# Kernel tuning notes

Measured on AMD Instinct MI355X. Metric: run time of the kernel, lower is better.

The kernel has to match this reference:

```python
import jax, jax.numpy as jnp
import numpy as np

N = 131072
D = 512        # input_dim
H = 512        # hidden_dim
E = 10         # num_experts
INIT_STD_SCALE = 0.1


def _trunc_normal(key, shape, std):
    # approximate trunc_normal_(std=std) in [-2std, 2std]
    return jnp.clip(jax.random.normal(key, shape) * std, -2.0 * std, 2.0 * std).astype(jnp.float32)


def setup_inputs() -> dict:
    key = jax.random.key(0)
    ks = jax.random.split(key, 6)
    x = jax.random.normal(ks[0], (N, D), dtype=jnp.float32)
    # router (default nn.Linear init approximated with uniform)
    lim = 1.0 / np.sqrt(D)
    Wr = jax.random.uniform(ks[1], (E, D), minval=-lim, maxval=lim, dtype=jnp.float32)
    br = jnp.zeros((E,), dtype=jnp.float32)
    # experts: trunc_normal with std = 0.1 / sqrt(fan_in), zero bias
    W1 = _trunc_normal(ks[2], (E, D, H), INIT_STD_SCALE / np.sqrt(D))   # [E, D, H]
    b1 = jnp.zeros((E, H), dtype=jnp.float32)
    W2 = _trunc_normal(ks[3], (E, H, H), INIT_STD_SCALE / np.sqrt(H))   # [E, H, H]
    b2 = jnp.zeros((E, H), dtype=jnp.float32)
    return {"x": x, "Wr": Wr, "br": br, "W1": W1, "b1": b1, "W2": W2, "b2": b2}


def reference(x, Wr, br, W1, b1, W2, b2):
    # router in fp32 (autocast disabled in original)
    logits = x.astype(jnp.float32) @ Wr.T + br          # [N, E]
    expert_ids = jnp.argmax(logits, axis=1)              # [N]
    out = jnp.zeros((x.shape[0], W2.shape[-1]), dtype=x.dtype)
    # fixed small loop over experts; dropout is identity at inference
    for e in range(W1.shape[0]):
        h = jax.nn.relu(x @ W1[e] + b1[e])                # [N, H]
        o = h @ W2[e] + b2[e]                             # [N, H]
        out = jnp.where((expert_ids == e)[:, None], o, out)
    return out, expert_ids
```

## Files before the change

### kernel.cpp

```cpp
#include <hip/hip_runtime.h>
#include <hip/hip_bf16.h>

#define N_TOK 131072
#define DIM   512
#define HID   512
#define NEXP  10

using bf16x8 = __attribute__((ext_vector_type(8))) short;
using f32x4  = __attribute__((ext_vector_type(4))) float;

__device__ __forceinline__ short f2bf(float f) {
    union { float f; unsigned u; } v; v.f = f;
    unsigned u = v.u;
    return (short)((u + 0x7FFFu + ((u >> 16) & 1u)) >> 16);
}

#define GLOAD16(g, l) __builtin_amdgcn_global_load_lds( \
    (const __attribute__((address_space(1))) void*)(g),  \
    (__attribute__((address_space(3))) void*)(l), 16, 0, 0)

__global__ __launch_bounds__(256) void router_kernel(
    const float* __restrict__ x, const float* __restrict__ Wr,
    const float* __restrict__ br, int* __restrict__ eid,
    float* __restrict__ ids_out, int* __restrict__ counts,
    short* __restrict__ xb)
{
    __shared__ float wr[NEXP][DIM];
    __shared__ int lcnt[NEXP];
    int tid = threadIdx.x;
    for (int i = tid; i < NEXP * DIM / 4; i += 256)
        ((float4*)wr)[i] = ((const float4*)Wr)[i];
    if (tid < NEXP) lcnt[tid] = 0;
    __syncthreads();

    int lane  = tid & 63;
    int wave  = tid >> 6;
    int gwave = blockIdx.x * 4 + wave;
    int nwav  = gridDim.x * 4;

    for (int t = gwave; t < N_TOK; t += nwav) {
        const float4* xr = (const float4*)(x + (size_t)t * DIM);
        float4 v0 = xr[lane * 2], v1 = xr[lane * 2 + 1];
        float xf[8] = {v0.x, v0.y, v0.z, v0.w, v1.x, v1.y, v1.z, v1.w};
        bf16x8 p;
        #pragma unroll
        for (int j = 0; j < 8; ++j) p[j] = f2bf(xf[j]);
        *(bf16x8*)(xb + (size_t)t * DIM + lane * 8) = p;

        float dot[NEXP];
        #pragma unroll
        for (int e = 0; e < NEXP; ++e) {
            const float* wv = &wr[e][lane * 8];
            float s = 0.f;
            #pragma unroll
            for (int j = 0; j < 8; ++j) s = fmaf(xf[j], wv[j], s);
            dot[e] = s;
        }
        #pragma unroll
        for (int off = 32; off > 0; off >>= 1) {
            #pragma unroll
            for (int e = 0; e < NEXP; ++e) dot[e] += __shfl_xor(dot[e], off, 64);
        }
        if (lane == 0) {
            int best = 0; float bv = dot[0] + br[0];
            #pragma unroll
            for (int e = 1; e < NEXP; ++e) {
                float v = dot[e] + br[e];
                if (v > bv) { bv = v; best = e; }
            }
            eid[t] = best;
            ids_out[t] = (float)best;
            atomicAdd(&lcnt[best], 1);
        }
    }
    __syncthreads();
    if (tid < NEXP) atomicAdd(&counts[tid], lcnt[tid]);
}

__global__ void offsets_kernel(const int* __restrict__ counts,
                               int* __restrict__ offsets, int* __restrict__ toff)
{
    if (threadIdx.x == 0) {
        int acc = 0, ta = 0;
        for (int e = 0; e < NEXP; ++e) {
            offsets[e] = acc; toff[e] = ta;
            acc += counts[e]; ta += (counts[e] + 127) >> 7;
        }
        offsets[NEXP] = acc; toff[NEXP] = ta;
    }
}

__global__ __launch_bounds__(256) void scatter_kernel(
    const int* __restrict__ eid, const int* __restrict__ offsets,
    int* __restrict__ cursors, int* __restrict__ perm)
{
    __shared__ int lcnt[NEXP], lbase[NEXP];
    int tid = threadIdx.x;
    if (tid < NEXP) lcnt[tid] = 0;
    __syncthreads();
    int t = blockIdx.x * 256 + tid;
    int e = 0, lpos = 0;
    if (t < N_TOK) {
        e = eid[t];
        lpos = atomicAdd(&lcnt[e], 1);
    }
    __syncthreads();
    if (tid < NEXP) lbase[tid] = atomicAdd(&cursors[tid], lcnt[tid]);
    __syncthreads();
    if (t < N_TOK) perm[offsets[e] + lbase[e] + lpos] = t;
}

__global__ __launch_bounds__(256) void wconvert_kernel(
    const float* __restrict__ W1, const float* __restrict__ W2,
    short* __restrict__ W1b, short* __restrict__ W2b)
{
    int mat = blockIdx.z;
    const float* src = (mat < NEXP) ? W1 + (size_t)mat * 512 * 512
                                    : W2 + (size_t)(mat - NEXP) * 512 * 512;
    short* dst = (mat < NEXP) ? W1b + (size_t)mat * 512 * 512
                              : W2b + (size_t)(mat - NEXP) * 512 * 512;
    __shared__ float tile[64][65];
    int r0 = blockIdx.y * 64, c0 = blockIdx.x * 64;
    int tid = threadIdx.x;
    int tr = tid >> 4, tc4 = (tid & 15) * 4;
    #pragma unroll
    for (int i = 0; i < 4; ++i) {
        float4 v = *(const float4*)(src + (size_t)(r0 + i * 16 + tr) * 512 + c0 + tc4);
        tile[i * 16 + tr][tc4 + 0] = v.x; tile[i * 16 + tr][tc4 + 1] = v.y;
        tile[i * 16 + tr][tc4 + 2] = v.z; tile[i * 16 + tr][tc4 + 3] = v.w;
    }
    __syncthreads();
    int s   = (r0 + tc4) >> 5;
    int kin = (r0 + tc4) & 31;
    #pragma unroll
    for (int i = 0; i < 4; ++i) {
        int cc = i * 16 + tr;
        ushort4 o;
        o.x = (ushort)f2bf(tile[tc4 + 0][cc]); o.y = (ushort)f2bf(tile[tc4 + 1][cc]);
        o.z = (ushort)f2bf(tile[tc4 + 2][cc]); o.w = (ushort)f2bf(tile[tc4 + 3][cc]);
        *(ushort4*)(dst + (size_t)s * 16384 + (size_t)(c0 + cc) * 32 + kin) = o;
    }
}

template<int LAYER>
__global__ __launch_bounds__(512, 4) void expert_gemm(
    const short* __restrict__ xb, const short* __restrict__ hA,
    const short* __restrict__ WT, const float* __restrict__ bias,
    const int* __restrict__ offsets, const int* __restrict__ toff,
    const int* __restrict__ perm,
    short* __restrict__ hOut, float* __restrict__ out)
{
    int g = blockIdx.x;
    if (g >= toff[NEXP]) return;
    int e = 0;
    #pragma unroll
    for (int k = 1; k < NEXP; ++k) e += (g >= toff[k]);
    int beg = offsets[e], cnt = offsets[e + 1] - beg;
    int m0 = (g - toff[e]) * 128;
    int nb = blockIdx.y * 256;

    __shared__ int toks[128];
    __shared__ short Ab[2][128 * 32];
    __shared__ short Bb[2][256 * 32];

    int tid = threadIdx.x, lane = tid & 63, w = tid >> 6;
    if (tid < 128) toks[tid] = perm[beg + min(m0 + tid, cnt - 1)];
    __syncthreads();

    const short* WTe = WT + (size_t)e * 512 * 512;
    int srow = w * 16 + (lane >> 2);
    int kqp  = lane & 3;
    int ql   = kqp ^ ((srow >> 1) & 3);
    const short* aS;
    if (LAYER == 1) aS = xb + (size_t)toks[srow] * DIM + ql * 8;
    else            aS = hA + (size_t)(beg + min(m0 + srow, cnt - 1)) * HID + ql * 8;
    const short* bS = WTe + (size_t)(nb + srow) * 32 + ql * 8;

    auto stage = [&](int t, int b) {
        GLOAD16(bS + t * 16384,        (char*)&Bb[b][0] + w * 1024);
        GLOAD16(bS + t * 16384 + 4096, (char*)&Bb[b][0] + 8192 + w * 1024);
        GLOAD16(aS + t * 32,           (char*)&Ab[b][0] + w * 1024);
    };

    int wr = w >> 2, wc = w & 3, lrow = lane & 15, kq = lane >> 4;
    int offA[4], offB[4];
    #pragma unroll
    for (int i = 0; i < 4; ++i) {
        int r = wr * 64 + i * 16 + lrow;
        offA[i] = r * 64 + (kq ^ ((r >> 1) & 3)) * 16;
    }
    #pragma unroll
    for (int j = 0; j < 4; ++j) {
        int r = wc * 64 + j * 16 + lrow;
        offB[j] = r * 64 + (kq ^ ((r >> 1) & 3)) * 16;
    }

    f32x4 acc[4][4];
    #pragma unroll
    for (int i = 0; i < 4; ++i)
        #pragma unroll
        for (int j = 0; j < 4; ++j) acc[i][j] = (f32x4){0.f, 0.f, 0.f, 0.f};

    auto comp = [&](int b) {
        bf16x8 af[4], bv[4];
        #pragma unroll
        for (int i = 0; i < 4; ++i) af[i] = *(const bf16x8*)((char*)&Ab[b][0] + offA[i]);
        #pragma unroll
        for (int j = 0; j < 4; ++j) bv[j] = *(const bf16x8*)((char*)&Bb[b][0] + offB[j]);
        __builtin_amdgcn_s_setprio(1);
        #pragma unroll
        for (int i = 0; i < 4; ++i)
            #pragma unroll
            for (int j = 0; j < 4; ++j)
                acc[i][j] = __builtin_amdgcn_mfma_f32_16x16x32_bf16(af[i], bv[j], acc[i][j], 0, 0, 0);
        __builtin_amdgcn_s_setprio(0);
    };

    stage(0, 0);
    stage(1, 1);
    asm volatile("s_waitcnt vmcnt(3)" ::: "memory");
    __builtin_amdgcn_s_barrier();

    #pragma unroll
    for (int t = 0; t < 16; ++t) {
        comp(t & 1);
        if (t == 15) break;
        __builtin_amdgcn_s_barrier();
        asm volatile("" ::: "memory");
        if (t + 2 < 16) {
            stage(t + 2, t & 1);
            asm volatile("s_waitcnt vmcnt(3)" ::: "memory");
        } else {
            asm volatile("s_waitcnt vmcnt(0)" ::: "memory");
        }
        __builtin_amdgcn_s_barrier();
    }

    const float* be = bias + (size_t)e * 512;
    int colb = nb + wc * 64 + lrow;
    float bvv[4];
    #pragma unroll
    for (int j = 0; j < 4; ++j) bvv[j] = be[colb + j * 16];

    #pragma unroll
    for (int i = 0; i < 4; ++i) {
        #pragma unroll
        for (int q = 0; q < 4; ++q) {
            int rr = wr * 64 + i * 16 + kq * 4 + q;
            if (m0 + rr < cnt) {
                if (LAYER == 1) {
                    short* hp = hOut + (size_t)(beg + m0 + rr) * HID + colb;
                    #pragma unroll
                    for (int j = 0; j < 4; ++j) {
                        float v = acc[i][j][q] + bvv[j];
                        hp[j * 16] = f2bf(v > 0.f ? v : 0.f);
                    }
                } else {
                    float* op = out + (size_t)toks[rr] * HID + colb;
                    #pragma unroll
                    for (int j = 0; j < 4; ++j)
                        op[j * 16] = acc[i][j][q] + bvv[j];
                }
            }
        }
    }
}

extern "C" void kernel_launch(void* const* d_in, const int* in_sizes, int n_in,
                              void* d_out, int out_size, void* d_ws, size_t ws_size,
                              hipStream_t stream)
{
    const float* x  = (const float*)d_in[0];
    const float* Wr = (const float*)d_in[1];
    const float* br = (const float*)d_in[2];
    const float* W1 = (const float*)d_in[3];
    const float* b1 = (const float*)d_in[4];
    const float* W2 = (const float*)d_in[5];
    const float* b2 = (const float*)d_in[6];

    float* out     = (float*)d_out;
    float* ids_out = out + (size_t)N_TOK * HID;

    char* ws     = (char*)d_ws;
    int* counts  = (int*)ws;
    int* offsets = counts + 16;
    int* toff    = counts + 32;
    int* cursors = counts + 48;
    int* eid     = (int*)(ws + 1024);
    int* perm    = eid + N_TOK;
    short* W1b   = (short*)(ws + 1024 + (size_t)2 * N_TOK * 4);
    short* W2b   = W1b + (size_t)NEXP * 512 * 512;
    short* h     = W2b + (size_t)NEXP * 512 * 512;
    short* xb    = h   + (size_t)N_TOK * HID;

    hipMemsetAsync(d_ws, 0, 1024, stream);
    router_kernel<<<2048, 256, 0, stream>>>(x, Wr, br, eid, ids_out, counts, xb);
    wconvert_kernel<<<dim3(8, 8, 2 * NEXP), 256, 0, stream>>>(W1, W2, W1b, W2b);
    offsets_kernel<<<1, 64, 0, stream>>>(counts, offsets, toff);
    scatter_kernel<<<512, 256, 0, stream>>>(eid, offsets, cursors, perm);

    int ntiles = (N_TOK + 127) / 128 + NEXP;
    expert_gemm<1><<<dim3(ntiles, 2), 512, 0, stream>>>(xb, nullptr, W1b, b1, offsets, toff, perm, h, nullptr);
    expert_gemm<2><<<dim3(ntiles, 2), 512, 0, stream>>>(nullptr, h, W2b, b2, offsets, toff, perm, nullptr, out);
}
```

Baseline: 366.5 us.

## Fuse both expert GEMM layers into one kernel keeping hidden tile in LDS

Replaces the two per-layer expert GEMM launches with a single fused kernel. Each block computes a 128-token by 256-column slice of the hidden activation, writes it after bias and ReLU into swizzled shared memory, and immediately uses it as the A operand for the second GEMM. Two output accumulator sets cover all 512 output columns. This removes the global write and re-read of the bf16 hidden tensor. The cost is about 112KB of shared memory per block, three accumulator sets raising register pressure (launch bounds drop to 2 blocks per CU), and half as many blocks in the grid. Layer-1 x tiles are also reloaded once per hidden half.

```diff
diff --git a/kernel.cpp b/kernel.cpp
--- a/kernel.cpp
+++ b/kernel.cpp
@@ -142,13 +142,12 @@
     }
 }
 
-template<int LAYER>
-__global__ __launch_bounds__(512, 4) void expert_gemm(
-    const short* __restrict__ xb, const short* __restrict__ hA,
-    const short* __restrict__ WT, const float* __restrict__ bias,
+__global__ __launch_bounds__(512, 2) void expert_fused(
+    const short* __restrict__ xb, const short* __restrict__ W1b,
+    const short* __restrict__ W2b, const float* __restrict__ b1,
+    const float* __restrict__ b2,
     const int* __restrict__ offsets, const int* __restrict__ toff,
-    const int* __restrict__ perm,
-    short* __restrict__ hOut, float* __restrict__ out)
+    const int* __restrict__ perm, float* __restrict__ out)
 {
     int g = blockIdx.x;
     if (g >= toff[NEXP]) return;
@@ -157,37 +156,32 @@
     for (int k = 1; k < NEXP; ++k) e += (g >= toff[k]);
     int beg = offsets[e], cnt = offsets[e + 1] - beg;
     int m0 = (g - toff[e]) * 128;
-    int nb = blockIdx.y * 256;
-
-    __shared__ int toks[128];
-    __shared__ short Ab[2][128 * 32];
-    __shared__ short Bb[2][256 * 32];
+
+    __shared__ char SMEM[114688 + 512];
+    #define ABOF(b) ((b) * 8192)
+    #define BBOF(b) (16384 + (b) * 16384)
+    #define HOFF    49152
 
     int tid = threadIdx.x, lane = tid & 63, w = tid >> 6;
+    int* toks = (int*)(SMEM + 114688);
     if (tid < 128) toks[tid] = perm[beg + min(m0 + tid, cnt - 1)];
     __syncthreads();
 
-    const short* WTe = WT + (size_t)e * 512 * 512;
-    int srow = w * 16 + (lane >> 2);
-    int kqp  = lane & 3;
+    const short* W1e = W1b + (size_t)e * 512 * 512;
+    const short* W2e = W2b + (size_t)e * 512 * 512;
+    int srow = tid >> 2;
+    int kqp  = tid & 3;
     int ql   = kqp ^ ((srow >> 1) & 3);
-    const short* aS;
-    if (LAYER == 1) aS = xb + (size_t)toks[srow] * DIM + ql * 8;
-    else            aS = hA + (size_t)(beg + min(m0 + srow, cnt - 1)) * HID + ql * 8;
-    const short* bS = WTe + (size_t)(nb + srow) * 32 + ql * 8;
-
-    auto stage = [&](int t, int b) {
-        GLOAD16(bS + t * 16384,        (char*)&Bb[b][0] + w * 1024);
-        GLOAD16(bS + t * 16384 + 4096, (char*)&Bb[b][0] + 8192 + w * 1024);
-        GLOAD16(aS + t * 32,           (char*)&Ab[b][0] + w * 1024);
-    };
+    const short* aS = xb + (size_t)toks[srow] * DIM + ql * 8;
 
     int wr = w >> 2, wc = w & 3, lrow = lane & 15, kq = lane >> 4;
-    int offA[4], offB[4];
+    int offA[4], offB[4], hbase[4], hxor[4];
     #pragma unroll
     for (int i = 0; i < 4; ++i) {
         int r = wr * 64 + i * 16 + lrow;
-        offA[i] = r * 64 + (kq ^ ((r >> 1) & 3)) * 16;
+        offA[i]  = r * 64 + (kq ^ ((r >> 1) & 3)) * 16;
+        hbase[i] = HOFF + r * 512;
+        hxor[i]  = r & 7;
     }
     #pragma unroll
     for (int j = 0; j < 4; ++j) {
@@ -195,75 +189,147 @@
         offB[j] = r * 64 + (kq ^ ((r >> 1) & 3)) * 16;
     }
 
-    f32x4 acc[4][4];
+    f32x4 accL[4][4], accP0[4][4], accP1[4][4];
     #pragma unroll
     for (int i = 0; i < 4; ++i)
         #pragma unroll
-        for (int j = 0; j < 4; ++j) acc[i][j] = (f32x4){0.f, 0.f, 0.f, 0.f};
-
-    auto comp = [&](int b) {
-        bf16x8 af[4], bv[4];
-        #pragma unroll
-        for (int i = 0; i < 4; ++i) af[i] = *(const bf16x8*)((char*)&Ab[b][0] + offA[i]);
-        #pragma unroll
-        for (int j = 0; j < 4; ++j) bv[j] = *(const bf16x8*)((char*)&Bb[b][0] + offB[j]);
-        __builtin_amdgcn_s_setprio(1);
+        for (int j = 0; j < 4; ++j) {
+            accP0[i][j] = (f32x4){0.f, 0.f, 0.f, 0.f};
+            accP1[i][j] = (f32x4){0.f, 0.f, 0.f, 0.f};
+        }
+
+    auto phaseAC = [&](int nb) {
         #pragma unroll
         for (int i = 0; i < 4; ++i)
             #pragma unroll
-            for (int j = 0; j < 4; ++j)
-                acc[i][j] = __builtin_amdgcn_mfma_f32_16x16x32_bf16(af[i], bv[j], acc[i][j], 0, 0, 0);
-        __builtin_amdgcn_s_setprio(0);
+            for (int j = 0; j < 4; ++j) accL[i][j] = (f32x4){0.f, 0.f, 0.f, 0.f};
+
+        auto stage = [&](int t, int b) {
+            const short* bs = W1e + (size_t)t * 16384 + (size_t)(nb + srow) * 32 + ql * 8;
+            GLOAD16(bs,        SMEM + BBOF(b) + tid * 16);
+            GLOAD16(bs + 4096, SMEM + BBOF(b) + 8192 + tid * 16);
+            GLOAD16(aS + t * 32, SMEM + ABOF(b) + tid * 16);
+        };
+        auto comp = [&](int b) {
+            bf16x8 af[4], bv[4];
+            #pragma unroll
+            for (int i = 0; i < 4; ++i) af[i] = *(const bf16x8*)(SMEM + ABOF(b) + offA[i]);
+            #pragma unroll
+            for (int j = 0; j < 4; ++j) bv[j] = *(const bf16x8*)(SMEM + BBOF(b) + offB[j]);
+            __builtin_amdgcn_s_setprio(1);
+            #pragma unroll
+            for (int i = 0; i < 4; ++i)
+                #pragma unroll
+                for (int j = 0; j < 4; ++j)
+                    accL[i][j] = __builtin_amdgcn_mfma_f32_16x16x32_bf16(af[i], bv[j], accL[i][j], 0, 0, 0);
+            __builtin_amdgcn_s_setprio(0);
+        };
+
+        stage(0, 0); stage(1, 1);
+        asm volatile("s_waitcnt vmcnt(3)" ::: "memory");
+        __builtin_amdgcn_s_barrier();
+        #pragma unroll
+        for (int t = 0; t < 16; ++t) {
+            comp(t & 1);
+            if (t == 15) break;
+            __builtin_amdgcn_s_barrier();
+            if (t + 2 < 16) {
+                stage(t + 2, t & 1);
+                asm volatile("s_waitcnt vmcnt(3)" ::: "memory");
+            } else {
+                asm volatile("s_waitcnt vmcnt(0)" ::: "memory");
+            }
+            __builtin_amdgcn_s_barrier();
+        }
+        const float* b1e = b1 + (size_t)e * 512 + nb;
+        float bvv[4];
+        #pragma unroll
+        for (int j = 0; j < 4; ++j) bvv[j] = b1e[wc * 64 + j * 16 + lrow];
+        #pragma unroll
+        for (int i = 0; i < 4; ++i)
+            #pragma unroll
+            for (int q = 0; q < 4; ++q) {
+                int row = wr * 64 + i * 16 + kq * 4 + q;
+                #pragma unroll
+                for (int j = 0; j < 4; ++j) {
+                    int col = wc * 64 + j * 16 + lrow;
+                    float v = accL[i][j][q] + bvv[j];
+                    v = v > 0.f ? v : 0.f;
+                    int slot = (col >> 3) ^ (row & 7);
+                    *(short*)(SMEM + HOFF + row * 512 + slot * 16 + (col & 7) * 2) = f2bf(v);
+                }
+            }
+        __syncthreads();
     };
 
-    stage(0, 0);
-    stage(1, 1);
-    asm volatile("s_waitcnt vmcnt(3)" ::: "memory");
-    __builtin_amdgcn_s_barrier();
-
-    #pragma unroll
-    for (int t = 0; t < 16; ++t) {
-        comp(t & 1);
-        if (t == 15) break;
+    auto phaseBD = [&](int ktbase, int nb2, f32x4 (&acc)[4][4]) {
+        auto stage = [&](int kt, int b) {
+            const short* bs = W2e + (size_t)kt * 16384 + (size_t)(nb2 + srow) * 32 + ql * 8;
+            GLOAD16(bs,        SMEM + BBOF(b) + tid * 16);
+            GLOAD16(bs + 4096, SMEM + BBOF(b) + 8192 + tid * 16);
+        };
+        auto comp = [&](int b, int t) {
+            bf16x8 af[4], bv[4];
+            #pragma unroll
+            for (int i = 0; i < 4; ++i)
+                af[i] = *(const bf16x8*)(SMEM + hbase[i] + (((t * 4 + kq) ^ hxor[i]) << 4));
+            #pragma unroll
+            for (int j = 0; j < 4; ++j) bv[j] = *(const bf16x8*)(SMEM + BBOF(b) + offB[j]);
+            __builtin_amdgcn_s_setprio(1);
+            #pragma unroll
+            for (int i = 0; i < 4; ++i)
+                #pragma unroll
+                for (int j = 0; j < 4; ++j)
+                    acc[i][j] = __builtin_amdgcn_mfma_f32_16x16x32_bf16(af[i], bv[j], acc[i][j], 0, 0, 0);
+            __builtin_amdgcn_s_setprio(0);
+        };
+
+        stage(ktbase + 0, 0); stage(ktbase + 1, 1);
+        asm volatile("s_waitcnt vmcnt(2)" ::: "memory");
         __builtin_amdgcn_s_barrier();
-        asm volatile("" ::: "memory");
-        if (t + 2 < 16) {
-            stage(t + 2, t & 1);
-            asm volatile("s_waitcnt vmcnt(3)" ::: "memory");
-        } else {
-            asm volatile("s_waitcnt vmcnt(0)" ::: "memory");
-        }
-        __builtin_amdgcn_s_barrier();
-    }
-
-    const float* be = bias + (size_t)e * 512;
-    int colb = nb + wc * 64 + lrow;
-    float bvv[4];
-    #pragma unroll
-    for (int j = 0; j < 4; ++j) bvv[j] = be[colb + j * 16];
-
+        #pragma unroll
+        for (int t = 0; t < 8; ++t) {
+            comp(t & 1, t);
+            if (t == 7) break;
+            __builtin_amdgcn_s_barrier();
+            if (t + 2 < 8) {
+                stage(ktbase + t + 2, t & 1);
+                asm volatile("s_waitcnt vmcnt(2)" ::: "memory");
+            } else {
+                asm volatile("s_waitcnt vmcnt(0)" ::: "memory");
+            }
+            __builtin_amdgcn_s_barrier();
+        }
+        __syncthreads();
+    };
+
+    phaseAC(0);
+    phaseBD(0, 0,   accP0);
+    phaseBD(0, 256, accP1);
+    phaseAC(256);
+    phaseBD(8, 0,   accP0);
+    phaseBD(8, 256, accP1);
+
+    const float* b2e = b2 + (size_t)e * 512;
     #pragma unroll
     for (int i = 0; i < 4; ++i) {
         #pragma unroll
         for (int q = 0; q < 4; ++q) {
             int rr = wr * 64 + i * 16 + kq * 4 + q;
             if (m0 + rr < cnt) {
-                if (LAYER == 1) {
-                    short* hp = hOut + (size_t)(beg + m0 + rr) * HID + colb;
-                    #pragma unroll
-                    for (int j = 0; j < 4; ++j) {
-                        float v = acc[i][j][q] + bvv[j];
-                        hp[j * 16] = f2bf(v > 0.f ? v : 0.f);
-                    }
-                } else {
-                    float* op = out + (size_t)toks[rr] * HID + colb;
-                    #pragma unroll
-                    for (int j = 0; j < 4; ++j)
-                        op[j * 16] = acc[i][j][q] + bvv[j];
+                float* op = out + (size_t)toks[rr] * HID;
+                int c0 = wc * 64 + lrow;
+                #pragma unroll
+                for (int j = 0; j < 4; ++j) {
+                    op[c0 + j * 16]       = accP0[i][j][q] + b2e[c0 + j * 16];
+                    op[256 + c0 + j * 16] = accP1[i][j][q] + b2e[256 + c0 + j * 16];
                 }
             }
         }
     }
+    #undef ABOF
+    #undef BBOF
+    #undef HOFF
 }
 
 extern "C" void kernel_launch(void* const* d_in, const int* in_sizes, int n_in,
@@ -290,8 +356,7 @@
     int* perm    = eid + N_TOK;
     short* W1b   = (short*)(ws + 1024 + (size_t)2 * N_TOK * 4);
     short* W2b   = W1b + (size_t)NEXP * 512 * 512;
-    short* h     = W2b + (size_t)NEXP * 512 * 512;
-    short* xb    = h   + (size_t)N_TOK * HID;
+    short* xb    = W2b + (size_t)NEXP * 512 * 512;
 
     hipMemsetAsync(d_ws, 0, 1024, stream);
     router_kernel<<<2048, 256, 0, stream>>>(x, Wr, br, eid, ids_out, counts, xb);
@@ -300,6 +365,6 @@
     scatter_kernel<<<512, 256, 0, stream>>>(eid, offsets, cursors, perm);
 
     int ntiles = (N_TOK + 127) / 128 + NEXP;
-    expert_gemm<1><<<dim3(ntiles, 2), 512, 0, stream>>>(xb, nullptr, W1b, b1, offsets, toff, perm, h, nullptr);
-    expert_gemm<2><<<dim3(ntiles, 2), 512, 0, stream>>>(nullptr, h, W2b, b2, offsets, toff, perm, nullptr, out);
-}
+    expert_fused<<<ntiles, 512, 0, stream>>>(xb, W1b, W2b, b1, b2,
+                                             offsets, toff, perm, out);
+}
```

New measurement: 461.2 us. +25.8%, slower.
